# Kernel tuning notes

Measured on AMD Instinct MI355X. Metric: run time of the kernel, lower is better.

Reference implementation:

```python
import jax, jax.numpy as jnp
import numpy as np

B, S, D, H = 2, 2048, 2048, 16
HD = D // H
ROPE_BASE = 10000.0
N_DOCS = 8


def setup_inputs() -> dict:
    key = jax.random.key(0)
    ks = jax.random.split(key, 7)
    scale = 1.0 / np.sqrt(D)
    x = jax.random.normal(ks[0], (B, S, D), dtype=jnp.float32)
    doc_ids = jnp.sort(jax.random.randint(ks[1], (B, S), 0, N_DOCS), axis=1)
    Wq = jax.random.normal(ks[2], (D, D), dtype=jnp.float32) * scale
    Wk = jax.random.normal(ks[3], (D, D), dtype=jnp.float32) * scale
    Wv = jax.random.normal(ks[4], (D, D), dtype=jnp.float32) * scale
    Wo = jax.random.normal(ks[5], (D, D), dtype=jnp.float32) * scale
    bo = jax.random.normal(ks[6], (D,), dtype=jnp.float32) * 0.01
    return {"x": x, "doc_ids": doc_ids, "Wq": Wq, "Wk": Wk, "Wv": Wv, "Wo": Wo, "bo": bo}


def _rotate_half(t):
    # interleaved pairs: (x0,x1,x2,x3,...) -> (-x1,x0,-x3,x2,...)
    t1 = t[..., 0::2]
    t2 = t[..., 1::2]
    return jnp.stack((-t2, t1), axis=-1).reshape(t.shape)


def _doc_position_ids(doc_ids):
    b, s = doc_ids.shape
    boundary = jnp.concatenate(
        [jnp.ones((b, 1), dtype=bool), doc_ids[:, 1:] != doc_ids[:, :-1]], axis=1)
    ar = jnp.arange(s)[None, :]
    boundary_pos = jnp.where(boundary, ar, 0)
    last_boundary = jax.lax.cummax(boundary_pos, axis=1)
    return ar - last_boundary  # position within each document


def reference(x, doc_ids, Wq, Wk, Wv, Wo, bo):
    b, s, d = x.shape
    h, hd = H, HD

    q = (x @ Wq).reshape(b, s, h, hd).transpose(0, 2, 1, 3)  # [b,h,s,hd]
    k = (x @ Wk).reshape(b, s, h, hd).transpose(0, 2, 1, 3)
    v = (x @ Wv).reshape(b, s, h, hd).transpose(0, 2, 1, 3)

    # doc-aware RoPE: positions reset at document boundaries
    pos = _doc_position_ids(doc_ids).astype(jnp.float32)  # [b,s]
    inv_freq = 1.0 / (ROPE_BASE ** (jnp.arange(0, hd, 2, dtype=jnp.float32) / hd))
    freqs = pos[..., None] * inv_freq  # [b,s,hd/2]
    cos = jnp.repeat(jnp.cos(freqs), 2, axis=-1)[:, None]  # [b,1,s,hd]
    sin = jnp.repeat(jnp.sin(freqs), 2, axis=-1)[:, None]
    q = q * cos + _rotate_half(q) * sin
    k = k * cos + _rotate_half(k) * sin

    scores = jnp.einsum("bhqd,bhkd->bhqk", q, k)
    # doc-blockwise causal mask: attend only to j<=i within same document
    same_doc = doc_ids[:, :, None] == doc_ids[:, None, :]  # [b,s,s] (i,j)
    allowed = jnp.tril(same_doc)[:, None]  # [b,1,s,s]
    inv_scale = 1.0 / np.sqrt(hd)
    scores = jnp.where(allowed, scores * inv_scale, -jnp.inf)
    attn = jax.nn.softmax(scores, axis=-1)

    ctx = jnp.einsum("bhqk,bhkd->bhqd", attn, v)
    ctx = ctx.transpose(0, 2, 1, 3).reshape(b, s, d)
    return ctx @ Wo + bo
```

## Files before the change

kernel.cpp:

```cpp
#include <hip/hip_runtime.h>
#include <hip/hip_bf16.h>

#define Dd 2048
#define Ss 2048
#define Bb 2
#define Hh 16
#define HDd 128
#define BSs (Bb*Ss)
#define NTIL 32

typedef __bf16 bf16;
typedef __bf16 bf16x8 __attribute__((ext_vector_type(8)));
typedef __bf16 bf16x4 __attribute__((ext_vector_type(4)));
typedef float f32x4 __attribute__((ext_vector_type(4)));

__device__ __forceinline__ void gload_lds16(const void* g, void* l) {
  __builtin_amdgcn_global_load_lds((__attribute__((address_space(1))) void*)(g),
                                   (__attribute__((address_space(3))) void*)(l), 16, 0, 0);
}

template <int N>
__device__ __forceinline__ void waitv() {
  if constexpr (N == 0) asm volatile("s_waitcnt vmcnt(0)" ::: "memory");
  else if constexpr (N == 6) asm volatile("s_waitcnt vmcnt(6)" ::: "memory");
}

__global__ void k_prep(const float* __restrict__ x, bf16* __restrict__ xb,
                       const float* __restrict__ Wq, const float* __restrict__ Wk,
                       const float* __restrict__ Wv, const float* __restrict__ Wo,
                       bf16* __restrict__ wqkvt, bf16* __restrict__ wot,
                       const int* __restrict__ doc, int* __restrict__ pos) {
  __shared__ char smem[16640];
  int zz = blockIdx.z;
  int tid = threadIdx.x;

  if (zz == 4) {
    int id = blockIdx.y * 32 + blockIdx.x;
    size_t base = (size_t)id * 8192 + tid * 4;
#pragma unroll
    for (int it = 0; it < 8; it++) {
      size_t i = base + (size_t)it * 1024;
      f32x4 v = *(const f32x4*)(x + i);
      bf16x4 o;
      o[0] = (bf16)v[0]; o[1] = (bf16)v[1]; o[2] = (bf16)v[2]; o[3] = (bf16)v[3];
      *(bf16x4*)(xb + i) = o;
    }
    return;
  }

  if (zz == 5) {
    if (blockIdx.x >= Bb || blockIdx.y != 0) return;
    int b = blockIdx.x;
    int* bp = (int*)smem;
    const int* db = doc + (size_t)b * Ss;
    for (int i = tid; i < Ss; i += 256) {
      int bd = (i == 0) || (db[i] != db[i - 1]);
      bp[i] = bd ? i : 0;
    }
    __syncthreads();
    int src = 0;
    for (int off = 1; off < Ss; off <<= 1) {
      for (int i = tid; i < Ss; i += 256) {
        int v = bp[src * Ss + i];
        if (i >= off) v = max(v, bp[src * Ss + i - off]);
        bp[(1 - src) * Ss + i] = v;
      }
      __syncthreads();
      src = 1 - src;
    }
    for (int i = tid; i < Ss; i += 256)
      pos[(size_t)b * Ss + i] = i - bp[src * Ss + i];
    return;
  }

  float (*t)[65] = (float(*)[65])smem;
  const float* W = (zz == 0) ? Wq : (zz == 1) ? Wk : (zz == 2) ? Wv : Wo;
  bf16* T = (zz < 3) ? (wqkvt + (size_t)zz * Dd * Dd) : wot;
  int n0 = blockIdx.x * 64, k0 = blockIdx.y * 64;
#pragma unroll
  for (int rr = 0; rr < 4; rr++) {
    int r = (tid >> 4) + rr * 16;
    f32x4 vv = *(const f32x4*)(W + (size_t)(k0 + r) * Dd + n0 + (tid & 15) * 4);
#pragma unroll
    for (int j = 0; j < 4; j++) t[r][(tid & 15) * 4 + j] = vv[j];
  }
  __syncthreads();
#pragma unroll
  for (int rr = 0; rr < 4; rr++) {
    int n = rr * 16 + (tid >> 4);
    int kb = (tid & 15) * 4;
    bf16x4 o;
#pragma unroll
    for (int j = 0; j < 4; j++) o[j] = (bf16)t[kb + j][n];
    *(bf16x4*)(T + (size_t)(n0 + n) * Dd + k0 + kb) = o;
  }
}

__device__ __forceinline__ void stage64(const char* gA, const char* gB,
                                        int m0, int n0, int t, int buf,
                                        char* AL, char* BL, int tid) {
  int ktb = t * 128;
#pragma unroll
  for (int p = 0; p < 2; p++) {
    int o = p * 8192 + tid * 16;
    int r = o >> 7, cb = o & 127;
    gload_lds16(gA + (size_t)(m0 + r) * 4096 + ktb + (cb ^ ((r & 7) << 4)),
                AL + buf * 16384 + o);
  }
#pragma unroll
  for (int p = 0; p < 4; p++) {
    int o = p * 8192 + tid * 16;
    int r = o >> 7, cb = o & 127;
    gload_lds16(gB + (size_t)(n0 + r) * 4096 + ktb + (cb ^ ((r & 7) << 4)),
                BL + buf * 32768 + o);
  }
}

template <bool STAGE, int WV>
__device__ __forceinline__ void do_tile64(const char* gA, const char* gB, int m0, int n0,
                                          int t, int bi, int b2, char* AL, char* BL, int tid,
                                          int wr, int wc, int ln, int g,
                                          f32x4 (&acc)[4][4]) {
  if (STAGE) stage64(gA, gB, m0, n0, t + 2, b2, AL, BL, tid);
  const char* tA = AL + bi * 16384;
  const char* tB = BL + bi * 32768;
#pragma unroll
  for (int kk = 0; kk < 2; kk++) {
    bf16x8 af[4], bf[4];
#pragma unroll
    for (int mq = 0; mq < 4; mq++) {
      int row = wr * 64 + mq * 16 + ln;
      af[mq] = *(const bf16x8*)(tA + row * 128 + ((kk * 64 + g * 16) ^ ((row & 7) << 4)));
    }
#pragma unroll
    for (int nq = 0; nq < 4; nq++) {
      int row = wc * 64 + nq * 16 + ln;
      bf[nq] = *(const bf16x8*)(tB + row * 128 + ((kk * 64 + g * 16) ^ ((row & 7) << 4)));
    }
    __builtin_amdgcn_s_setprio(1);
#pragma unroll
    for (int mq = 0; mq < 4; mq++)
#pragma unroll
      for (int nq = 0; nq < 4; nq++)
        acc[mq][nq] = __builtin_amdgcn_mfma_f32_16x16x32_bf16(af[mq], bf[nq], acc[mq][nq], 0, 0, 0);
    __builtin_amdgcn_s_setprio(0);
  }
  waitv<WV>();
  __builtin_amdgcn_s_barrier();
}

__device__ __forceinline__ void gemm64_core(const bf16* gA_, const bf16* gB_,
                                            int m0, int n0, char* AL, char* BL,
                                            f32x4 (&acc)[4][4]) {
  const char* gA = (const char*)gA_;
  const char* gB = (const char*)gB_;
  const int tid = threadIdx.x;
  const int l = tid & 63, w = tid >> 6;
  const int wr = w >> 2, wc = w & 3;
  const int g = l >> 4, ln = l & 15;
  f32x4 z = {0.f, 0.f, 0.f, 0.f};
#pragma unroll
  for (int i = 0; i < 4; i++)
#pragma unroll
    for (int n = 0; n < 4; n++) acc[i][n] = z;

  stage64(gA, gB, m0, n0, 0, 0, AL, BL, tid);
  stage64(gA, gB, m0, n0, 1, 1, AL, BL, tid);
  waitv<6>();
  __builtin_amdgcn_s_barrier();

  for (int tt = 0; tt < 10; tt++) {
    int t = tt * 3;
    do_tile64<true, 6>(gA, gB, m0, n0, t,     0, 2, AL, BL, tid, wr, wc, ln, g, acc);
    do_tile64<true, 6>(gA, gB, m0, n0, t + 1, 1, 0, AL, BL, tid, wr, wc, ln, g, acc);
    do_tile64<true, 6>(gA, gB, m0, n0, t + 2, 2, 1, AL, BL, tid, wr, wc, ln, g, acc);
  }
  do_tile64<false, 0>(gA, gB, m0, n0, 30, 0, 0, AL, BL, tid, wr, wc, ln, g, acc);
  do_tile64<false, -1>(gA, gB, m0, n0, 31, 1, 0, AL, BL, tid, wr, wc, ln, g, acc);
}

__global__ __launch_bounds__(512, 2) void k_qkv256(const bf16* __restrict__ xb,
                                                   const bf16* __restrict__ wqkvt,
                                                   const int* __restrict__ pos,
                                                   bf16* __restrict__ q,
                                                   bf16* __restrict__ k,
                                                   bf16* __restrict__ vt) {
  __shared__ char SLM[147456];
  char* AL = SLM;
  char* BL = SLM + 49152;
  int bid = blockIdx.x;
  int x = bid & 7, j = bid >> 3;
  int mt = j / 3, nt = x * 3 + (j % 3);
  int m0 = mt * 128, n0 = nt * 256;

  f32x4 acc[4][4];
  gemm64_core(xb, wqkvt, m0, n0, AL, BL, acc);

  const int tid = threadIdx.x;
  const int l = tid & 63, w = tid >> 6;
  const int wr = w >> 2, wc = w & 3, g = l >> 4, ln = l & 15;
  int z = n0 >> 11;
  int n0l = n0 & 2047;
  int bix = m0 >> 11;
  int sl0 = m0 & 2047;

  if (z == 2) {
#pragma unroll
    for (int mq = 0; mq < 4; mq++) {
      int sl = sl0 + wr * 64 + mq * 16 + g * 4;
#pragma unroll
      for (int nq = 0; nq < 4; nq++) {
        int col = n0l + wc * 64 + nq * 16 + ln;
        int h = col >> 7, hd = col & 127;
        bf16x4 o;
#pragma unroll
        for (int r2 = 0; r2 < 4; r2++) o[r2] = (bf16)acc[mq][nq][r2];
        *(bf16x4*)(vt + (((size_t)(bix * Hh + h) * HDd + hd) * Ss + sl)) = o;
      }
    }
  } else {
    bf16* dst = (z == 0) ? q : k;
    float* T = (float*)SLM;
    const float c1 = 0.14391156642398168f;
    int cg = (tid & 31) * 8;
    int hb = n0l + cg;
    int hh = hb >> 7, hd0 = hb & 127;
    float fr[4];
#pragma unroll
    for (int pr = 0; pr < 4; pr++)
      fr[pr] = __expf(-(float)((hd0 >> 1) + pr) * c1);

#pragma unroll
    for (int pass = 0; pass < 2; pass++) {
      __syncthreads();
      if (wr == pass) {
#pragma unroll
        for (int mq = 0; mq < 4; mq++) {
#pragma unroll
          for (int nq = 0; nq < 4; nq++) {
            int c = wc * 64 + nq * 16 + ln;
            int rb = mq * 16 + g * 4;
#pragma unroll
            for (int r2 = 0; r2 < 4; r2++)
              T[(rb + r2) * 260 + c] = acc[mq][nq][r2];
          }
        }
      }
      __syncthreads();
#pragma unroll
      for (int j2 = 0; j2 < 4; j2++) {
        int r = j2 * 16 + (tid >> 5);
        int sg = m0 + pass * 64 + r;
        float p = (float)pos[sg];
        f32x4 v0 = *(const f32x4*)(T + r * 260 + cg);
        f32x4 v1 = *(const f32x4*)(T + r * 260 + cg + 4);
        float e0[4] = {v0[0], v0[2], v1[0], v1[2]};
        float e1[4] = {v0[1], v0[3], v1[1], v1[3]};
        int s = sg & 2047;
        bf16x8 o;
#pragma unroll
        for (int pr = 0; pr < 4; pr++) {
          float ang = p * fr[pr];
          float sn, cs;
          __sincosf(ang, &sn, &cs);
          o[2 * pr]     = (bf16)(e0[pr] * cs - e1[pr] * sn);
          o[2 * pr + 1] = (bf16)(e1[pr] * cs + e0[pr] * sn);
        }
        *(bf16x8*)(dst + (((size_t)(bix * Hh + hh) * Ss + s) * HDd + hd0)) = o;
      }
    }
  }
}

__global__ __launch_bounds__(512, 2) void k_out256(const bf16* __restrict__ ctx,
                                                   const bf16* __restrict__ wot,
                                                   const float* __restrict__ bo,
                                                   float* __restrict__ outp) {
  __shared__ char AL[49152];
  __shared__ char BL[98304];
  int bid = blockIdx.x;
  int x = bid & 7, j = bid >> 3;
  int mt = j, nt = x;
  int m0 = mt * 128, n0 = nt * 256;

  f32x4 acc[4][4];
  gemm64_core(ctx, wot, m0, n0, AL, BL, acc);

  const int l = threadIdx.x & 63, w = threadIdx.x >> 6;
  const int wr = w >> 2, wc = w & 3, g = l >> 4, ln = l & 15;
  float bov[4];
#pragma unroll
  for (int nq = 0; nq < 4; nq++)
    bov[nq] = bo[n0 + wc * 64 + nq * 16 + ln];
#pragma unroll
  for (int mq = 0; mq < 4; mq++)
#pragma unroll
    for (int r2 = 0; r2 < 4; r2++) {
      int row = m0 + wr * 64 + mq * 16 + g * 4 + r2;
#pragma unroll
      for (int nq = 0; nq < 4; nq++) {
        int col = n0 + wc * 64 + nq * 16 + ln;
        outp[(size_t)row * Dd + col] = acc[mq][nq][r2] + bov[nq];
      }
    }
}

__global__ __launch_bounds__(256) void k_attn(const bf16* __restrict__ q,
                                              const bf16* __restrict__ k,
                                              const bf16* __restrict__ vt,
                                              const int* __restrict__ pos,
                                              bf16* __restrict__ ctx) {
  __shared__ bf16 Ks[64 * 128];
  __shared__ bf16 Vts[128 * 64];
  __shared__ bf16 Pw[4][16 * 64];
  int bid = blockIdx.x;
  int xc = bid & 7, jj = bid >> 3;
  int bh = xc * 4 + (jj >> 5);
  int idx5 = jj & 31;
  int qt = (idx5 & 1) ? (31 - (idx5 >> 1)) : (idx5 >> 1);
  int b = bh >> 4, h = bh & 15;
  int q0 = qt * 64;
  const int tid = threadIdx.x, l = tid & 63, w = tid >> 6, g = l >> 4, ln = l & 15;
  const bf16* qb = q + (size_t)bh * Ss * HDd;
  const bf16* kb = k + (size_t)bh * Ss * HDd;
  const bf16* vb = vt + (size_t)bh * Ss * HDd;

  bf16x8 qf[4];
  int qr = q0 + w * 16 + ln;
#pragma unroll
  for (int ks = 0; ks < 4; ks++)
    qf[ks] = *(const bf16x8*)(qb + (size_t)qr * HDd + ks * 32 + 8 * g);

  int rrow[4], dstart[4];
  float m[4], lsum[4];
#pragma unroll
  for (int r2 = 0; r2 < 4; r2++) {
    rrow[r2] = q0 + w * 16 + 4 * g + r2;
    dstart[r2] = rrow[r2] - pos[(size_t)b * Ss + rrow[r2]];
    m[r2] = -1e30f;
    lsum[r2] = 0.f;
  }
  f32x4 oacc[8];
  f32x4 z = {0.f, 0.f, 0.f, 0.f};
#pragma unroll
  for (int n = 0; n < 8; n++) oacc[n] = z;

  int kt_start = (q0 - pos[(size_t)b * Ss + q0]) >> 6;
  const float iscale = 0.08838834764831845f;

  for (int kt = kt_start; kt <= qt; kt++) {
    int kv0 = kt * 64;
#pragma unroll
    for (int i2 = 0; i2 < 4; i2++) {
      int o = i2 * 4096 + w * 1024 + l * 16;
      int rk = o >> 8, cbk = o & 255;
      gload_lds16((const char*)kb + (size_t)(kv0 + rk) * 256 + cbk,
                  (char*)Ks + i2 * 4096 + w * 1024);
      int rv = o >> 7, cbv = o & 127;
      gload_lds16((const char*)vb + (size_t)rv * (Ss * 2) + (size_t)kv0 * 2 + cbv,
                  (char*)Vts + i2 * 4096 + w * 1024);
    }
    __syncthreads();

    f32x4 sc[4];
#pragma unroll
    for (int n = 0; n < 4; n++) {
      f32x4 a = z;
#pragma unroll
      for (int ks = 0; ks < 4; ks++) {
        bf16x8 bfrag = *(const bf16x8*)(Ks + (n * 16 + ln) * 128 + ks * 32 + 8 * g);
        a = __builtin_amdgcn_mfma_f32_16x16x32_bf16(qf[ks], bfrag, a, 0, 0, 0);
      }
      sc[n] = a;
    }

    float pmax[4] = {-1e30f, -1e30f, -1e30f, -1e30f};
    float pv[4][4];
#pragma unroll
    for (int n = 0; n < 4; n++) {
      int kvc = kv0 + n * 16 + ln;
#pragma unroll
      for (int r2 = 0; r2 < 4; r2++) {
        bool ok = (kvc <= rrow[r2]) && (kvc >= dstart[r2]);
        float sv = ok ? sc[n][r2] * iscale : -1e30f;
        pv[n][r2] = sv;
        pmax[r2] = fmaxf(pmax[r2], sv);
      }
    }
#pragma unroll
    for (int off = 1; off < 16; off <<= 1)
#pragma unroll
      for (int r2 = 0; r2 < 4; r2++)
        pmax[r2] = fmaxf(pmax[r2], __shfl_xor(pmax[r2], off, 64));

    float alpha[4];
#pragma unroll
    for (int r2 = 0; r2 < 4; r2++) {
      float mn = fmaxf(m[r2], pmax[r2]);
      alpha[r2] = __expf(m[r2] - mn);
      m[r2] = mn;
    }

    float rs[4] = {0.f, 0.f, 0.f, 0.f};
#pragma unroll
    for (int n = 0; n < 4; n++) {
      int kvc = kv0 + n * 16 + ln;
#pragma unroll
      for (int r2 = 0; r2 < 4; r2++) {
        bool ok = (kvc <= rrow[r2]) && (kvc >= dstart[r2]);
        float p = ok ? __expf(pv[n][r2] - m[r2]) : 0.f;
        rs[r2] += p;
        Pw[w][(4 * g + r2) * 64 + n * 16 + ln] = (bf16)p;
      }
    }
#pragma unroll
    for (int off = 1; off < 16; off <<= 1)
#pragma unroll
      for (int r2 = 0; r2 < 4; r2++) rs[r2] += __shfl_xor(rs[r2], off, 64);
#pragma unroll
    for (int r2 = 0; r2 < 4; r2++) lsum[r2] = lsum[r2] * alpha[r2] + rs[r2];
#pragma unroll
    for (int n = 0; n < 8; n++)
#pragma unroll
      for (int r2 = 0; r2 < 4; r2++) oacc[n][r2] *= alpha[r2];
    __syncthreads();

#pragma unroll
    for (int n = 0; n < 8; n++) {
#pragma unroll
      for (int ks = 0; ks < 2; ks++) {
        bf16x8 pa = *(const bf16x8*)(&Pw[w][ln * 64 + ks * 32 + 8 * g]);
        bf16x8 vfr = *(const bf16x8*)(Vts + (n * 16 + ln) * 64 + ks * 32 + 8 * g);
        oacc[n] = __builtin_amdgcn_mfma_f32_16x16x32_bf16(pa, vfr, oacc[n], 0, 0, 0);
      }
    }
    __syncthreads();
  }

#pragma unroll
  for (int n = 0; n < 8; n++)
#pragma unroll
    for (int r2 = 0; r2 < 4; r2++) {
      float val = oacc[n][r2] / lsum[r2];
      ctx[((size_t)(b * Ss + rrow[r2])) * Dd + h * HDd + n * 16 + ln] = (bf16)val;
    }
}

extern "C" void kernel_launch(void* const* d_in, const int* in_sizes, int n_in,
                              void* d_out, int out_size, void* d_ws, size_t ws_size,
                              hipStream_t stream) {
  const float* x = (const float*)d_in[0];
  const int* doc = (const int*)d_in[1];
  const float* Wq = (const float*)d_in[2];
  const float* Wk = (const float*)d_in[3];
  const float* Wv = (const float*)d_in[4];
  const float* Wo = (const float*)d_in[5];
  const float* bo = (const float*)d_in[6];
  float* outp = (float*)d_out;

  char* ws = (char*)d_ws;
  size_t off = 0;
  auto alloc = [&](size_t bytes) {
    char* p = ws + off;
    off += (bytes + 255) & ~(size_t)255;
    return p;
  };
  bf16* xb = (bf16*)alloc((size_t)BSs * Dd * 2);
  bf16* wqkvt = (bf16*)alloc((size_t)3 * Dd * Dd * 2);
  bf16* wot = (bf16*)alloc((size_t)Dd * Dd * 2);
  bf16* qd = (bf16*)alloc((size_t)BSs * Dd * 2);
  bf16* kd = (bf16*)alloc((size_t)BSs * Dd * 2);
  bf16* vtd = (bf16*)alloc((size_t)BSs * Dd * 2);
  bf16* ctxd = (bf16*)alloc((size_t)BSs * Dd * 2);
  int* pos = (int*)alloc((size_t)BSs * 4);

  k_prep<<<dim3(32, 32, 6), 256, 0, stream>>>(x, xb, Wq, Wk, Wv, Wo, wqkvt, wot, doc, pos);
  k_qkv256<<<dim3(768), 512, 0, stream>>>(xb, wqkvt, pos, qd, kd, vtd);
  k_attn<<<dim3(1024), 256, 0, stream>>>(qd, kd, vtd, pos, ctxd);
  k_out256<<<dim3(256), 512, 0, stream>>>(ctxd, wot, bo, outp);
}
```

Before: 215.9 us.

## Replace QKV GEMM with 256x256-tile kernel using fine-grained half-tile staging

```diff
diff --git a/kernel.cpp b/kernel.cpp
--- a/kernel.cpp
+++ b/kernel.cpp
@@ -22,6 +22,8 @@
 template <int N>
 __device__ __forceinline__ void waitv() {
   if constexpr (N == 0) asm volatile("s_waitcnt vmcnt(0)" ::: "memory");
+  else if constexpr (N == 2) asm volatile("s_waitcnt vmcnt(2)" ::: "memory");
+  else if constexpr (N == 4) asm volatile("s_waitcnt vmcnt(4)" ::: "memory");
   else if constexpr (N == 6) asm volatile("s_waitcnt vmcnt(6)" ::: "memory");
 }
 
@@ -93,6 +95,255 @@
 #pragma unroll
     for (int j = 0; j < 4; j++) o[j] = (bf16)t[kb + j][n];
     *(bf16x4*)(T + (size_t)(n0 + n) * Dd + k0 + kb) = o;
+  }
+}
+
+__device__ __forceinline__ bf16x8 rd8(const char* base, int lr, int cb) {
+  return *(const bf16x8*)(base + lr * 128 + (cb ^ ((lr & 7) << 4)));
+}
+
+__device__ __forceinline__ void stage_half8(const char* g, int rbase, int ktb, char* lds, int tid) {
+#pragma unroll
+  for (int p = 0; p < 2; p++) {
+    int o = p * 8192 + tid * 16;
+    int r = o >> 7, cb = o & 127;
+    gload_lds16(g + (size_t)(rbase + r) * 4096 + ktb + (cb ^ ((r & 7) << 4)), lds + o);
+  }
+}
+
+template <int MB, int NB>
+__device__ __forceinline__ void quad(f32x4 (&acc)[8][4], bf16x8 (&A)[4][2], bf16x8 (&B)[2][2]) {
+  __builtin_amdgcn_s_setprio(1);
+#pragma unroll
+  for (int mq = 0; mq < 4; mq++)
+#pragma unroll
+    for (int nq = 0; nq < 2; nq++)
+#pragma unroll
+      for (int kk = 0; kk < 2; kk++)
+        acc[MB + mq][NB + nq] = __builtin_amdgcn_mfma_f32_16x16x32_bf16(
+            A[mq][kk], B[nq][kk], acc[MB + mq][NB + nq], 0, 0, 0);
+  __builtin_amdgcn_s_setprio(0);
+}
+
+template <bool FULL>
+__device__ __forceinline__ void iter8(const char* gA, const char* gB, int m0, int n0,
+                                      int E, char* AL, char* BL, int tid,
+                                      int wr, int wc, int ln, int g, f32x4 (&acc)[8][4]) {
+  const int ktbO = E * 128 + 128, ktbN = E * 128 + 256, ktbN1 = E * 128 + 384;
+  const char* A0b = AL + wr * 16384;
+  const char* A1b = AL + 32768 + wr * 16384;
+  const char* B0b = BL + (wc >> 1) * 16384;
+  const char* B1b = BL + 32768 + (wc >> 1) * 16384;
+  const int lb = (wc & 1) * 64;
+  bf16x8 af[4][2], bfa[2][2], bfb[2][2];
+
+#pragma unroll
+  for (int mq = 0; mq < 4; mq++) {
+    int lr = mq * 16 + ln;
+#pragma unroll
+    for (int kk = 0; kk < 2; kk++) af[mq][kk] = rd8(A0b, lr, kk * 64 + g * 16);
+  }
+#pragma unroll
+  for (int nq = 0; nq < 2; nq++) {
+    int lr = lb + nq * 16 + ln;
+#pragma unroll
+    for (int kk = 0; kk < 2; kk++) bfa[nq][kk] = rd8(B0b, lr, kk * 64 + g * 16);
+  }
+  stage_half8(gA, m0, ktbO, AL + 32768, tid);
+  __builtin_amdgcn_s_barrier();
+  quad<0, 0>(acc, af, bfa);
+  __builtin_amdgcn_s_barrier();
+
+#pragma unroll
+  for (int nq = 0; nq < 2; nq++) {
+    int lr = lb + (2 + nq) * 16 + ln;
+#pragma unroll
+    for (int kk = 0; kk < 2; kk++) bfb[nq][kk] = rd8(B0b, lr, kk * 64 + g * 16);
+  }
+  stage_half8(gA, m0 + 128, ktbO, AL + 32768 + 16384, tid);
+  __builtin_amdgcn_s_barrier();
+  quad<0, 2>(acc, af, bfb);
+  __builtin_amdgcn_s_barrier();
+
+#pragma unroll
+  for (int mq = 0; mq < 4; mq++) {
+    int lr = 64 + mq * 16 + ln;
+#pragma unroll
+    for (int kk = 0; kk < 2; kk++) af[mq][kk] = rd8(A0b, lr, kk * 64 + g * 16);
+  }
+  if (FULL) stage_half8(gB, n0, ktbN, BL, tid);
+  __builtin_amdgcn_s_barrier();
+  quad<4, 0>(acc, af, bfa);
+  __builtin_amdgcn_s_barrier();
+
+  if (FULL) stage_half8(gB, n0 + 128, ktbN, BL + 16384, tid);
+  waitv<FULL ? 4 : 0>();
+  __builtin_amdgcn_s_barrier();
+  quad<4, 2>(acc, af, bfb);
+  __builtin_amdgcn_s_barrier();
+
+#pragma unroll
+  for (int mq = 0; mq < 4; mq++) {
+    int lr = mq * 16 + ln;
+#pragma unroll
+    for (int kk = 0; kk < 2; kk++) af[mq][kk] = rd8(A1b, lr, kk * 64 + g * 16);
+  }
+#pragma unroll
+  for (int nq = 0; nq < 2; nq++) {
+    int lr = lb + nq * 16 + ln;
+#pragma unroll
+    for (int kk = 0; kk < 2; kk++) bfa[nq][kk] = rd8(B1b, lr, kk * 64 + g * 16);
+  }
+  if (FULL) stage_half8(gA, m0, ktbN, AL, tid);
+  __builtin_amdgcn_s_barrier();
+  quad<0, 0>(acc, af, bfa);
+  __builtin_amdgcn_s_barrier();
+
+#pragma unroll
+  for (int nq = 0; nq < 2; nq++) {
+    int lr = lb + (2 + nq) * 16 + ln;
+#pragma unroll
+    for (int kk = 0; kk < 2; kk++) bfb[nq][kk] = rd8(B1b, lr, kk * 64 + g * 16);
+  }
+  if (FULL) stage_half8(gA, m0 + 128, ktbN, AL + 16384, tid);
+  __builtin_amdgcn_s_barrier();
+  quad<0, 2>(acc, af, bfb);
+  __builtin_amdgcn_s_barrier();
+
+#pragma unroll
+  for (int mq = 0; mq < 4; mq++) {
+    int lr = 64 + mq * 16 + ln;
+#pragma unroll
+    for (int kk = 0; kk < 2; kk++) af[mq][kk] = rd8(A1b, lr, kk * 64 + g * 16);
+  }
+  if (FULL) stage_half8(gB, n0, ktbN1, BL + 32768, tid);
+  __builtin_amdgcn_s_barrier();
+  quad<4, 0>(acc, af, bfa);
+  __builtin_amdgcn_s_barrier();
+
+  if (FULL) {
+    stage_half8(gB, n0 + 128, ktbN1, BL + 32768 + 16384, tid);
+    waitv<4>();
+  }
+  __builtin_amdgcn_s_barrier();
+  quad<4, 2>(acc, af, bfb);
+  __builtin_amdgcn_s_barrier();
+}
+
+__global__ __launch_bounds__(512, 2) void k_qkv8p(const bf16* __restrict__ xb,
+                                                  const bf16* __restrict__ wqkvt,
+                                                  const int* __restrict__ pos,
+                                                  bf16* __restrict__ q,
+                                                  bf16* __restrict__ k,
+                                                  bf16* __restrict__ vt) {
+  __shared__ char SLM[131072];
+  char* AL = SLM;
+  char* BL = SLM + 65536;
+  int bid = blockIdx.x;
+  int x = bid & 7, j = bid >> 3;
+  int mt = j / 3, nt = x * 3 + (j % 3);
+  int m0 = mt * 256, n0 = nt * 256;
+
+  const int tid = threadIdx.x;
+  const int l = tid & 63, w = tid >> 6;
+  const int wr = w >> 2, wc = w & 3;
+  const int g = l >> 4, ln = l & 15;
+
+  f32x4 acc[8][4];
+  f32x4 z = {0.f, 0.f, 0.f, 0.f};
+#pragma unroll
+  for (int i = 0; i < 8; i++)
+#pragma unroll
+    for (int n = 0; n < 4; n++) acc[i][n] = z;
+
+  const char* gA = (const char*)xb;
+  const char* gB = (const char*)wqkvt;
+
+  stage_half8(gA, m0, 0, AL, tid);
+  stage_half8(gA, m0 + 128, 0, AL + 16384, tid);
+  stage_half8(gB, n0, 0, BL, tid);
+  stage_half8(gB, n0 + 128, 0, BL + 16384, tid);
+  stage_half8(gB, n0, 128, BL + 32768, tid);
+  stage_half8(gB, n0 + 128, 128, BL + 32768 + 16384, tid);
+  waitv<4>();
+  __builtin_amdgcn_s_barrier();
+
+#pragma unroll 1
+  for (int jj = 0; jj < 15; jj++)
+    iter8<true>(gA, gB, m0, n0, 2 * jj, AL, BL, tid, wr, wc, ln, g, acc);
+  iter8<false>(gA, gB, m0, n0, 30, AL, BL, tid, wr, wc, ln, g, acc);
+
+  int zsec = n0 >> 11;
+  int n0l = n0 & 2047;
+  int bix = m0 >> 11;
+  int sl0 = m0 & 2047;
+
+  if (zsec == 2) {
+#pragma unroll
+    for (int mf = 0; mf < 8; mf++) {
+      int sl = sl0 + wr * 128 + mf * 16 + g * 4;
+#pragma unroll
+      for (int nf = 0; nf < 4; nf++) {
+        int col = n0l + wc * 64 + nf * 16 + ln;
+        int h = col >> 7, hd = col & 127;
+        bf16x4 o;
+#pragma unroll
+        for (int r2 = 0; r2 < 4; r2++) o[r2] = (bf16)acc[mf][nf][r2];
+        *(bf16x4*)(vt + (((size_t)(bix * Hh + h) * HDd + hd) * Ss + sl)) = o;
+      }
+    }
+  } else {
+    bf16* dst = (zsec == 0) ? q : k;
+    float* T = (float*)SLM;
+    const float c1 = 0.14391156642398168f;
+    int cg = (tid & 31) * 8;
+    int hb = n0l + cg;
+    int hh = hb >> 7, hd0 = hb & 127;
+    float fr[4];
+#pragma unroll
+    for (int pr = 0; pr < 4; pr++)
+      fr[pr] = __expf(-(float)((hd0 >> 1) + pr) * c1);
+
+#pragma unroll
+    for (int pass = 0; pass < 4; pass++) {
+      __syncthreads();
+      if (wr == (pass >> 1)) {
+#pragma unroll
+        for (int mq2 = 0; mq2 < 4; mq2++) {
+          int mf = (pass & 1) * 4 + mq2;
+#pragma unroll
+          for (int nf = 0; nf < 4; nf++) {
+            int c = wc * 64 + nf * 16 + ln;
+            int rb = mq2 * 16 + g * 4;
+#pragma unroll
+            for (int r2 = 0; r2 < 4; r2++)
+              T[(rb + r2) * 260 + c] = acc[mf][nf][r2];
+          }
+        }
+      }
+      __syncthreads();
+#pragma unroll
+      for (int j2 = 0; j2 < 4; j2++) {
+        int r = j2 * 16 + (tid >> 5);
+        int sg = m0 + pass * 64 + r;
+        float p = (float)pos[sg];
+        f32x4 v0 = *(const f32x4*)(T + r * 260 + cg);
+        f32x4 v1 = *(const f32x4*)(T + r * 260 + cg + 4);
+        float e0[4] = {v0[0], v0[2], v1[0], v1[2]};
+        float e1[4] = {v0[1], v0[3], v1[1], v1[3]};
+        int s = sg & 2047;
+        bf16x8 o;
+#pragma unroll
+        for (int pr = 0; pr < 4; pr++) {
+          float ang = p * fr[pr];
+          float sn, cs;
+          __sincosf(ang, &sn, &cs);
+          o[2 * pr]     = (bf16)(e0[pr] * cs - e1[pr] * sn);
+          o[2 * pr + 1] = (bf16)(e1[pr] * cs + e0[pr] * sn);
+        }
+        *(bf16x8*)(dst + (((size_t)(bix * Hh + hh) * Ss + s) * HDd + hd0)) = o;
+      }
+    }
   }
 }
 
@@ -177,99 +428,6 @@
   }
   do_tile64<false, 0>(gA, gB, m0, n0, 30, 0, 0, AL, BL, tid, wr, wc, ln, g, acc);
   do_tile64<false, -1>(gA, gB, m0, n0, 31, 1, 0, AL, BL, tid, wr, wc, ln, g, acc);
-}
-
-__global__ __launch_bounds__(512, 2) void k_qkv256(const bf16* __restrict__ xb,
-                                                   const bf16* __restrict__ wqkvt,
-                                                   const int* __restrict__ pos,
-                                                   bf16* __restrict__ q,
-                                                   bf16* __restrict__ k,
-                                                   bf16* __restrict__ vt) {
-  __shared__ char SLM[147456];
-  char* AL = SLM;
-  char* BL = SLM + 49152;
-  int bid = blockIdx.x;
-  int x = bid & 7, j = bid >> 3;
-  int mt = j / 3, nt = x * 3 + (j % 3);
-  int m0 = mt * 128, n0 = nt * 256;
-
-  f32x4 acc[4][4];
-  gemm64_core(xb, wqkvt, m0, n0, AL, BL, acc);
-
-  const int tid = threadIdx.x;
-  const int l = tid & 63, w = tid >> 6;
-  const int wr = w >> 2, wc = w & 3, g = l >> 4, ln = l & 15;
-  int z = n0 >> 11;
-  int n0l = n0 & 2047;
-  int bix = m0 >> 11;
-  int sl0 = m0 & 2047;
-
-  if (z == 2) {
-#pragma unroll
-    for (int mq = 0; mq < 4; mq++) {
-      int sl = sl0 + wr * 64 + mq * 16 + g * 4;
-#pragma unroll
-      for (int nq = 0; nq < 4; nq++) {
-        int col = n0l + wc * 64 + nq * 16 + ln;
-        int h = col >> 7, hd = col & 127;
-        bf16x4 o;
-#pragma unroll
-        for (int r2 = 0; r2 < 4; r2++) o[r2] = (bf16)acc[mq][nq][r2];
-        *(bf16x4*)(vt + (((size_t)(bix * Hh + h) * HDd + hd) * Ss + sl)) = o;
-      }
-    }
-  } else {
-    bf16* dst = (z == 0) ? q : k;
-    float* T = (float*)SLM;
-    const float c1 = 0.14391156642398168f;
-    int cg = (tid & 31) * 8;
-    int hb = n0l + cg;
-    int hh = hb >> 7, hd0 = hb & 127;
-    float fr[4];
-#pragma unroll
-    for (int pr = 0; pr < 4; pr++)
-      fr[pr] = __expf(-(float)((hd0 >> 1) + pr) * c1);
-
-#pragma unroll
-    for (int pass = 0; pass < 2; pass++) {
-      __syncthreads();
-      if (wr == pass) {
-#pragma unroll
-        for (int mq = 0; mq < 4; mq++) {
-#pragma unroll
-          for (int nq = 0; nq < 4; nq++) {
-            int c = wc * 64 + nq * 16 + ln;
-            int rb = mq * 16 + g * 4;
-#pragma unroll
-            for (int r2 = 0; r2 < 4; r2++)
-              T[(rb + r2) * 260 + c] = acc[mq][nq][r2];
-          }
-        }
-      }
-      __syncthreads();
-#pragma unroll
-      for (int j2 = 0; j2 < 4; j2++) {
-        int r = j2 * 16 + (tid >> 5);
-        int sg = m0 + pass * 64 + r;
-        float p = (float)pos[sg];
-        f32x4 v0 = *(const f32x4*)(T + r * 260 + cg);
-        f32x4 v1 = *(const f32x4*)(T + r * 260 + cg + 4);
-        float e0[4] = {v0[0], v0[2], v1[0], v1[2]};
-        float e1[4] = {v0[1], v0[3], v1[1], v1[3]};
-        int s = sg & 2047;
-        bf16x8 o;
-#pragma unroll
-        for (int pr = 0; pr < 4; pr++) {
-          float ang = p * fr[pr];
-          float sn, cs;
-          __sincosf(ang, &sn, &cs);
-          o[2 * pr]     = (bf16)(e0[pr] * cs - e1[pr] * sn);
-          o[2 * pr + 1] = (bf16)(e1[pr] * cs + e0[pr] * sn);
-        }
-        *(bf16x8*)(dst + (((size_t)(bix * Hh + hh) * Ss + s) * HDd + hd0)) = o;
-      }
-    }
-  }
 }
 
 __global__ __launch_bounds__(512, 2) void k_out256(const bf16* __restrict__ ctx,
@@ -475,7 +633,7 @@
   int* pos = (int*)alloc((size_t)BSs * 4);
 
   k_prep<<<dim3(32, 32, 6), 256, 0, stream>>>(x, xb, Wq, Wk, Wv, Wo, wqkvt, wot, doc, pos);
-  k_qkv256<<<dim3(768), 512, 0, stream>>>(xb, wqkvt, pos, qd, kd, vtd);
+  k_qkv8p<<<dim3(384), 512, 0, stream>>>(xb, wqkvt, pos, qd, kd, vtd);
   k_attn<<<dim3(1024), 256, 0, stream>>>(qd, kd, vtd, pos, ctxd);
   k_out256<<<dim3(256), 512, 0, stream>>>(ctxd, wot, bo, outp);
 }
```

Measured after the change: 223.2 us. 1.03x slower.
